# Optimization experiments

Hardware: AMD Instinct MI355X
Metric: run time of the kernel (lower is better)

The kernel has to match this reference:

```python
import jax, jax.numpy as jnp
import numpy as np

NUM_HEADS = 16
HEAD_DIM = 64
HIDDEN = NUM_HEADS * HEAD_DIM  # 1024
MAX_POS = 1024


def setup_inputs() -> dict:
    key = jax.random.key(0)
    ks = jax.random.split(key, 6)
    B, L, H = 8, 1024, HIDDEN
    hidden_states = jax.random.normal(ks[0], (B, L, H), dtype=jnp.float32)
    attention_mask = jnp.zeros((B, 1, 1, L), dtype=jnp.float32)
    scale = 0.02  # keep pre-softmax logits in a sane range
    Wq = jax.random.normal(ks[1], (H, H), dtype=jnp.float32) * scale
    Wk = jax.random.normal(ks[2], (H, H), dtype=jnp.float32) * scale
    Wv = jax.random.normal(ks[3], (H, H), dtype=jnp.float32) * scale
    bq = jnp.zeros((H,), dtype=jnp.float32)
    bk = jnp.zeros((H,), dtype=jnp.float32)
    bv = jnp.zeros((H,), dtype=jnp.float32)
    dist_emb = jax.random.normal(ks[4], (2 * MAX_POS - 1, HEAD_DIM), dtype=jnp.float32) * scale
    return {"hidden_states": hidden_states, "attention_mask": attention_mask,
            "Wq": Wq, "bq": bq, "Wk": Wk, "bk": bk, "Wv": Wv, "bv": bv,
            "dist_emb": dist_emb}


def _split_heads(x):
    # [B, L, H] -> [B, nH, L, hd]
    B, L, _ = x.shape
    return x.reshape(B, L, NUM_HEADS, HEAD_DIM).transpose(0, 2, 1, 3)


def reference(hidden_states, attention_mask, Wq, bq, Wk, bk, Wv, bv, dist_emb):
    B, L, H = hidden_states.shape
    q = _split_heads(hidden_states @ Wq.T + bq)  # [B,h,L,d]
    k = _split_heads(hidden_states @ Wk.T + bk)
    v = _split_heads(hidden_states @ Wv.T + bv)

    scores = jnp.einsum("bhld,bhrd->bhlr", q, k)

    # relative_key_query positional bias
    pos_l = jnp.arange(L)[:, None]
    pos_r = jnp.arange(L)[None, :]
    dist_idx = pos_l - pos_r + MAX_POS - 1          # [L, L], in [0, 2*MAX_POS-2]
    pos_emb = dist_emb[dist_idx]                    # [L, L, d]
    scores = scores + jnp.einsum("bhld,lrd->bhlr", q, pos_emb)
    scores = scores + jnp.einsum("bhrd,lrd->bhlr", k, pos_emb)

    scores = scores / jnp.sqrt(jnp.float32(HEAD_DIM))
    scores = scores + attention_mask                # additive mask broadcast [B,1,1,L]
    probs = jax.nn.softmax(scores, axis=-1)         # dropout = identity (eval)
    ctx = jnp.einsum("bhlr,bhrd->bhld", probs, v)
    ctx = ctx.transpose(0, 2, 1, 3).reshape(B, L, H)
    return ctx
```

## Files before the change

kernel.cpp:

```cpp
#include <hip/hip_runtime.h>
#include <stdint.h>

typedef short s16x8 __attribute__((ext_vector_type(8)));
typedef float f32x4 __attribute__((ext_vector_type(4)));

#define MFMA16(a, b, c) __builtin_amdgcn_mfma_f32_16x16x32_bf16((a), (b), (c), 0, 0, 0)

__device__ __forceinline__ ushort f2b(float f) {
  union { float f; uint32_t u; } x; x.f = f;
  uint32_t r = x.u + 0x7fffu + ((x.u >> 16) & 1u);
  return (ushort)(r >> 16);
}
__device__ __forceinline__ float b2f(ushort s) {
  union { uint32_t u; float f; } x; x.u = ((uint32_t)s) << 16;
  return x.f;
}
__device__ __forceinline__ uint32_t pack2t(float a, float b) {
  return __builtin_amdgcn_perm(__float_as_uint(b), __float_as_uint(a), 0x07060302u);
}
__device__ __forceinline__ uint32_t cvtpk(float a, float b) {
  uint32_t r;
  asm("v_cvt_pk_bf16_f32 %0, %1, %2" : "=v"(r) : "v"(a), "v"(b));
  return r;
}

__global__ __launch_bounds__(256) void cast_f32_bf16(const float* __restrict__ src,
                                                     ushort* __restrict__ dst, int n) {
  int i = (blockIdx.x * 256 + threadIdx.x) * 4;
  if (i + 4 <= n) {
    float4 v = *(const float4*)(src + i);
    ushort4 o; o.x = f2b(v.x); o.y = f2b(v.y); o.z = f2b(v.z); o.w = f2b(v.w);
    *(ushort4*)(dst + i) = o;
  }
}

__device__ __forceinline__ void gload16(const void* g, void* l) {
  __builtin_amdgcn_global_load_lds((const __attribute__((address_space(1))) void*)g,
                                   (__attribute__((address_space(3))) void*)l, 16, 0, 0);
}

__global__ __launch_bounds__(256) void qkv_gemm(
    const ushort* __restrict__ hb, const ushort* __restrict__ wb,
    const float* __restrict__ bq, const float* __restrict__ bk, const float* __restrict__ bv,
    ushort* __restrict__ qb, ushort* __restrict__ kb, ushort* __restrict__ vt) {
  __shared__ ushort As[128 * 32];
  __shared__ ushort Bs[128 * 32];
  const int tid = threadIdx.x;
  const int w = tid >> 6, lane = tid & 63, quad = lane >> 4, l16 = lane & 15;
  const int m0 = blockIdx.y * 128, n0 = blockIdx.x * 128;

  const int srow = w * 32 + (lane >> 2);
  const int scol = (lane & 3) * 8;
  const ushort* ga = hb + (size_t)(m0 + srow) * 1024 + scol;
  const ushort* gw = wb + (size_t)(n0 + srow) * 1024 + scol;
  ushort* lA0 = As + (w * 32) * 32;
  ushort* lA1 = As + (w * 32 + 16) * 32;
  ushort* lB0 = Bs + (w * 32) * 32;
  ushort* lB1 = Bs + (w * 32 + 16) * 32;

  f32x4 acc[4][4];
#pragma unroll
  for (int mt = 0; mt < 4; ++mt)
#pragma unroll
    for (int nt = 0; nt < 4; ++nt) acc[mt][nt] = (f32x4){0.f, 0.f, 0.f, 0.f};

  const int wm = (w >> 1) * 64, wn = (w & 1) * 64;

  for (int k0 = 0; k0 < 1024; k0 += 32) {
    gload16(ga + k0, lA0);
    gload16(ga + k0 + 16 * 1024, lA1);
    gload16(gw + k0, lB0);
    gload16(gw + k0 + 16 * 1024, lB1);
    __syncthreads();
    s16x8 af[4], bfr[4];
#pragma unroll
    for (int mt = 0; mt < 4; ++mt)
      af[mt] = *(const s16x8*)(As + (wm + 16 * mt + l16) * 32 + quad * 8);
#pragma unroll
    for (int nt = 0; nt < 4; ++nt)
      bfr[nt] = *(const s16x8*)(Bs + (wn + 16 * nt + l16) * 32 + quad * 8);
#pragma unroll
    for (int mt = 0; mt < 4; ++mt)
#pragma unroll
      for (int nt = 0; nt < 4; ++nt)
        acc[mt][nt] = MFMA16(af[mt], bfr[nt], acc[mt][nt]);
    __syncthreads();
  }

  const int mat = n0 >> 10;
  const float* bias = (mat == 0) ? bq : ((mat == 1) ? bk : bv);
  const int b = m0 >> 10;
#pragma unroll
  for (int mt = 0; mt < 4; ++mt) {
    int mbase = m0 + wm + 16 * mt + 4 * quad;
#pragma unroll
    for (int nt = 0; nt < 4; ++nt) {
      int n = n0 + wn + 16 * nt + l16;
      int o = n & 1023; int hh = o >> 6; int d = o & 63;
      float bsv = bias[o];
#pragma unroll
      for (int reg = 0; reg < 4; ++reg) {
        int l = (mbase + reg) & 1023;
        ushort bx = f2b(acc[mt][nt][reg] + bsv);
        if (mat == 0)      qb[(((size_t)(b * 16 + hh)) * 1024 + l) * 64 + d] = bx;
        else if (mat == 1) kb[(((size_t)(b * 16 + hh)) * 1024 + l) * 64 + d] = bx;
        else               vt[(((size_t)(b * 16 + hh)) * 64 + d) * 1024 + l] = bx;
      }
    }
  }
}

#define KR  0
#define VR  8192
#define ER  16384
#define SER 28672
#define PR  35072

__global__ __launch_bounds__(256, 2) void attn_kernel(
    const ushort* __restrict__ qb, const ushort* __restrict__ kb,
    const ushort* __restrict__ vt, const ushort* __restrict__ eb,
    const float* __restrict__ mask, float* __restrict__ out) {
  __shared__ __align__(16) ushort sm[39168];
  const int tid = threadIdx.x;
  const int w = tid >> 6, lane = tid & 63, quad = lane >> 4, l16 = lane & 15;
  const int bh = blockIdx.y, b = bh >> 4, h = bh & 15;
  const int l0 = blockIdx.x * 64;

  const int srow = lane >> 3;
  const int colb = ((lane & 7) ^ srow) * 8;
  const int row0 = w * 8 + srow;

  const ushort* kp = kb + ((size_t)bh * 1024 + row0) * 64 + colb;
  const ushort* vp = vt + ((size_t)bh * 64 + row0) * 1024 + colb;
  const float* maskp = mask + b * 1024 + l16;

  const int p0 = blockIdx.x % 3;

  {
    const ushort* qp = qb + ((size_t)bh * 1024 + l0 + row0) * 64 + colb;
    gload16(qp,         sm + PR + w * 512);
    gload16(qp + 2048,  sm + PR + 2048 + w * 512);
    gload16(kp,         sm + KR + w * 512);
    gload16(kp + 2048,  sm + KR + 2048 + w * 512);
    gload16(vp,         sm + VR + w * 512);
    gload16(vp + 32768, sm + VR + 2048 + w * 512);
    const int t0i = l0 + 960;
#pragma unroll
    for (int c2 = 0; c2 < 4; ++c2) {
      int jb = w * 8 + 32 * c2;
      int seg = p0 + (jb >> 6); if (seg >= 3) seg -= 3;
      int t = t0i + jb + srow; if (t > 2046) t = 2046;
      gload16(eb + (size_t)t * 64 + colb, sm + ER + seg * 4096 + (jb & 63) * 64);
    }
  }

  const int lm7 = l16 & 7;
  const int swzq = (quad ^ lm7) * 8;
  int offR0[4], offR1[4];
#pragma unroll
  for (int nt = 0; nt < 4; ++nt) {
    offR0[nt] = (16 * nt + l16) * 64 + swzq;
    offR1[nt] = offR0[nt] ^ 32;
  }
  const int offW0 = (w * 16 + l16) * 64 + swzq;
  const int offW1 = offW0 ^ 32;
  const int offPW0 = PR + offW0, offPW1 = PR + offW1;
  int eoffA[5], eoffB[5]; bool selA[5], selB[5];
#pragma unroll
  for (int i = 0; i < 5; ++i) {
    int ba = w + i, bbk = 3 - w + i;
    eoffA[i] = ((ba & 3) * 16 + l16) * 64 + swzq;  selA[i] = (ba & 4) != 0;
    eoffB[i] = ((bbk & 3) * 16 + l16) * 64 + swzq; selB[i] = (bbk & 4) != 0;
  }
  int offSW[5];
#pragma unroll
  for (int i = 0; i < 5; ++i)
    offSW[i] = SER + w * 1600 + (16 * i + l16) * 20 + 4 * quad;
  const int bbF = SER + (w * 16 + 4 * quad + 15 - l16) * 20 + l16;
  int addrP[4][4];
#pragma unroll
  for (int nt = 0; nt < 4; ++nt)
#pragma unroll
    for (int reg = 0; reg < 4; ++reg)
      addrP[nt][reg] = PR + (w * 16 + 4 * quad + reg) * 64
                     + (((2 * nt + (l16 >> 3)) ^ ((4 * quad + reg) & 7)) * 8) + lm7;
  int bidx[4]; bool bcnd[4];
#pragma unroll
  for (int r = 0; r < 4; ++r) {
    bidx[r] = (quad * 16 + ((4 * quad + r + 15 - l16) & 15)) * 4;
    bcnd[r] = (4 * quad + r) > l16;
  }

  __syncthreads();

  const s16x8 aq0 = *(const s16x8*)(sm + offPW0);
  const s16x8 aq1 = *(const s16x8*)(sm + offPW1);

  float rsum[4];
  f32x4 o_acc[4];
#pragma unroll
  for (int r = 0; r < 4; ++r) rsum[r] = 0.f;
#pragma unroll
  for (int nt = 0; nt < 4; ++nt) o_acc[nt] = (f32x4){0.f, 0.f, 0.f, 0.f};
  const f32x4 ZACC = {0.f, 0.f, 0.f, 0.f};

  const float LOG2E = 1.44269504088896f;
  const float SC = 0.125f * LOG2E;

  int s0 = p0;

#define ATTN_ITER(P)                                                               \
  {                                                                                \
    const int it = 2 * ith + (P);                                                  \
    const int r0 = it * 64;                                                        \
    __syncthreads();      \
                   \
    {                                                                              \
      const int rn = (r0 + 64) & 1023;                                             \
      gload16(kp + rn * 64,        sm + KR + 4096 * (1 - (P)) + w * 512);          \
      gload16(kp + rn * 64 + 2048, sm + KR + 4096 * (1 - (P)) + 2048 + w * 512);   \
      gload16(vp + rn,             sm + VR + 4096 * (1 - (P)) + w * 512);          \
      gload16(vp + rn + 32768,     sm + VR + 4096 * (1 - (P)) + 2048 + w * 512);   \
      int pnew = s0 + 2; if (pnew >= 3) pnew -= 3;                                 \
      const int tb = l0 + 960 - r0 - 64;                                           \
      _Pragma("unroll")                                                            \
      for (int c2 = 0; c2 < 2; ++c2) {                                             \
        int o = w * 8 + 32 * c2;                                                   \
        int t = tb + o + srow; t = t < 0 ? 0 : (t > 2046 ? 2046 : t);              \
        gload16(eb + (size_t)t * 64 + colb, sm + ER + pnew * 4096 + o * 64);       \
      }                                                                            \
    }                                                                              \
    float mkv[4];                                                                  \
    _Pragma("unroll")                                                              \
    for (int nt = 0; nt < 4; ++nt) mkv[nt] = maskp[r0 + 16 * nt] * LOG2E;          \
    const int sA4 = s0 * 4096;                                                     \
    int sBi = s0 + 1; if (sBi >= 3) sBi -= 3;                                      \
    const int sB4 = sBi * 4096;                                                    \
    const ushort* KbP = sm + KR + 4096 * (P);                                      \
                         \
    __builtin_amdgcn_s_setprio(1);                                                 \
    f32x4 zv[4];                                                                   \
    _Pragma("unroll")                                                              \
    for (int nt = 0; nt < 4; ++nt) {                                               \
      s16x8 bk0 = *(const s16x8*)(KbP + offR0[nt]);                                \
      s16x8 bk1 = *(const s16x8*)(KbP + offR1[nt]);                                \
      f32x4 z = MFMA16(aq0, bk0, ZACC);                                            \
      zv[nt] = MFMA16(aq1, bk1, z);                                                \
    }                                                                              \
    const s16x8 ak0 = *(const s16x8*)(KbP + offW0);                                \
    const s16x8 ak1 = *(const s16x8*)(KbP + offW1);                                \
    f32x4 d1[5];                                                                   \
    _Pragma("unroll")                                                              \
    for (int i = 0; i < 5; ++i) {                                                  \
      int ea = (selA[i] ? sB4 : sA4) + eoffA[i];                                   \
      s16x8 be0 = *(const s16x8*)(sm + ER + ea);                                   \
      s16x8 be1 = *(const s16x8*)(sm + ER + (ea ^ 32));                            \
      f32x4 z = MFMA16(aq0, be0, ZACC);                                            \
      d1[i] = MFMA16(aq1, be1, z);                                                 \
    }                                                                              \
    __builtin_amdgcn_s_setprio(0);                                                 \
                                  \
    _Pragma("unroll")                                                              \
    for (int r = 0; r < 4; ++r) {                                                  \
      float bp[5];                                                                 \
      _Pragma("unroll")                                                            \
      for (int i = 0; i < 5; ++i)                                                  \
        bp[i] = __int_as_float(                                                    \
            __builtin_amdgcn_ds_bpermute(bidx[r], __float_as_int(d1[i][r])));      \
      _Pragma("unroll")                                                            \
      for (int nt = 0; nt < 4; ++nt)                                               \
        zv[nt][r] += bcnd[r] ? bp[4 - nt] : bp[3 - nt];                            \
    }                                                                              \
                               \
    __builtin_amdgcn_s_setprio(1);                                                 \
    _Pragma("unroll")                                                              \
    for (int i = 0; i < 5; ++i) {                                                  \
      int ea = (selB[i] ? sB4 : sA4) + eoffB[i];                                   \
      s16x8 be0 = *(const s16x8*)(sm + ER + ea);                                   \
      s16x8 be1 = *(const s16x8*)(sm + ER + (ea ^ 32));                            \
      f32x4 z = MFMA16(ak0, be0, ZACC);                                            \
      z = MFMA16(ak1, be1, z);                                                     \
      uint2 pk; pk.x = pack2t(z[0], z[1]); pk.y = pack2t(z[2], z[3]);              \
      *(uint2*)(sm + offSW[i]) = pk;                                               \
    }                                                                              \
    __builtin_amdgcn_s_setprio(0);                                                 \
    __syncthreads();                  \
                    \
    _Pragma("unroll")                                                              \
    for (int nt = 0; nt < 4; ++nt) {                                               \
      _Pragma("unroll")                                                            \
      for (int reg = 0; reg < 4; ++reg) {                                          \
        float z2 = (zv[nt][reg] + b2f(sm[bbF + nt * 1600 + reg * 20])) * SC        \
                 + mkv[nt];                                                        \
        float pe = exp2f(z2);                                                      \
        zv[nt][reg] = pe;                                                          \
        rsum[reg] += pe;                                                           \
      }                                                                            \
    }                                                                              \
               \
    _Pragma("unroll")                                                              \
    for (int nt = 0; nt < 4; ++nt) {                                               \
      uint32_t u01 = cvtpk(zv[nt][0], zv[nt][1]);                                  \
      uint32_t u23 = cvtpk(zv[nt][2], zv[nt][3]);                                  \
      sm[addrP[nt][0]] = (ushort)u01;                                              \
      sm[addrP[nt][1]] = (ushort)(u01 >> 16);                                      \
      sm[addrP[nt][2]] = (ushort)u23;                                              \
      sm[addrP[nt][3]] = (ushort)(u23 >> 16);                                      \
    }                                                                              \
       \
    __builtin_amdgcn_s_setprio(1);                                                 \
    {                                                                              \
      const ushort* VbP = sm + VR + 4096 * (P);                                    \
      const s16x8 ap0 = *(const s16x8*)(sm + offPW0);                              \
      _Pragma("unroll")                                                            \
      for (int nt = 0; nt < 4; ++nt) {                                             \
        s16x8 bv0 = *(const s16x8*)(VbP + offR0[nt]);                              \
        o_acc[nt] = MFMA16(ap0, bv0, o_acc[nt]);                                   \
      }                                                                            \
      const s16x8 ap1 = *(const s16x8*)(sm + offPW1);                              \
      _Pragma("unroll")                                                            \
      for (int nt = 0; nt < 4; ++nt) {                                             \
        s16x8 bv1 = *(const s16x8*)(VbP + offR1[nt]);                              \
        o_acc[nt] = MFMA16(ap1, bv1, o_acc[nt]);                                   \
      }                                                                            \
    }                                                                              \
    __builtin_amdgcn_s_setprio(0);                                                 \
    s0 = (s0 == 0) ? 2 : s0 - 1;                   \
  }

#pragma unroll 1
  for (int ith = 0; ith < 8; ++ith) {
    ATTN_ITER(0)
    ATTN_ITER(1)
  }
#undef ATTN_ITER

#pragma unroll
  for (int off = 1; off < 16; off <<= 1)
#pragma unroll
    for (int reg = 0; reg < 4; ++reg)
      rsum[reg] += __shfl_xor(rsum[reg], off);

#pragma unroll
  for (int nt = 0; nt < 4; ++nt)
#pragma unroll
    for (int reg = 0; reg < 4; ++reg) {
      int l = l0 + w * 16 + 4 * quad + reg;
      int d = 16 * nt + l16;
      out[((size_t)(b * 1024 + l)) * 1024 + h * 64 + d] = o_acc[nt][reg] / rsum[reg];
    }
}

extern "C" void kernel_launch(void* const* d_in, const int* in_sizes, int n_in,
                              void* d_out, int out_size, void* d_ws, size_t ws_size,
                              hipStream_t stream) {
  const float* hidden = (const float*)d_in[0];
  const float* mask   = (const float*)d_in[1];
  const float* Wq     = (const float*)d_in[2];
  const float* bq     = (const float*)d_in[3];
  const float* Wk     = (const float*)d_in[4];
  const float* bk     = (const float*)d_in[5];
  const float* Wv     = (const float*)d_in[6];
  const float* bv     = (const float*)d_in[7];
  const float* dist   = (const float*)d_in[8];
  float* out = (float*)d_out;

  ushort* ws = (ushort*)d_ws;
  ushort* qb = ws;
  ushort* kb = ws + 8388608;
  ushort* vt = ws + 16777216;
  ushort* hb = ws + 25165824;
  ushort* wb = ws + 33554432;
  ushort* eb = ws + 36700160;

  cast_f32_bf16<<<8192, 256, 0, stream>>>(hidden, hb, 8388608);
  cast_f32_bf16<<<1024, 256, 0, stream>>>(Wq, wb, 1048576);
  cast_f32_bf16<<<1024, 256, 0, stream>>>(Wk, wb + 1048576, 1048576);
  cast_f32_bf16<<<1024, 256, 0, stream>>>(Wv, wb + 2097152, 1048576);
  cast_f32_bf16<<<128, 256, 0, stream>>>(dist, eb, 131008);

  qkv_gemm<<<dim3(24, 64), 256, 0, stream>>>(hb, wb, bq, bk, bv, qb, kb, vt);
  attn_kernel<<<dim3(16, 128), 256, 0, stream>>>(qb, kb, vt, eb, mask, out);
}
```

Before: 382.7 us.

## Double-buffer QKV GEMM LDS tiles, use explicit waitcnt barriers, merge weight casts

The QKV GEMM now uses two LDS buffers, so the global-to-LDS load of the next K slice is issued before the MFMAs on the current slice. This overlaps load latency with compute. Barriers in the GEMM and attention kernels are replaced with explicit s_waitcnt vmcnt/lgkmcnt plus s_barrier, and the barrier at the first attention iteration is skipped. These barriers rely on the waits being correct for the async LDS loads. The three weight cast launches are merged into one kernel to cut launch overhead.

```diff
diff --git a/kernel.cpp b/kernel.cpp
--- a/kernel.cpp
+++ b/kernel.cpp
@@ -22,6 +22,17 @@
   uint32_t r;
   asm("v_cvt_pk_bf16_f32 %0, %1, %2" : "=v"(r) : "v"(a), "v"(b));
   return r;
+}
+
+__device__ __forceinline__ void barrier_vm() {
+  asm volatile("s_waitcnt vmcnt(0)" ::: "memory");
+  __builtin_amdgcn_s_barrier();
+  __builtin_amdgcn_sched_barrier(0);
+}
+__device__ __forceinline__ void barrier_lgkm() {
+  asm volatile("s_waitcnt lgkmcnt(0)" ::: "memory");
+  __builtin_amdgcn_s_barrier();
+  __builtin_amdgcn_sched_barrier(0);
 }
 
 __global__ __launch_bounds__(256) void cast_f32_bf16(const float* __restrict__ src,
@@ -34,6 +45,20 @@
   }
 }
 
+__global__ __launch_bounds__(256) void cast3_f32_bf16(
+    const float* __restrict__ a, const float* __restrict__ b,
+    const float* __restrict__ c, ushort* __restrict__ dst) {
+  int blk = blockIdx.x;
+  const float* src; int base;
+  if (blk < 1024)      { src = a; base = 0; }
+  else if (blk < 2048) { src = b; base = 1048576; blk -= 1024; }
+  else                 { src = c; base = 2097152; blk -= 2048; }
+  int i = (blk * 256 + threadIdx.x) * 4;
+  float4 v = *(const float4*)(src + i);
+  ushort4 o; o.x = f2b(v.x); o.y = f2b(v.y); o.z = f2b(v.z); o.w = f2b(v.w);
+  *(ushort4*)(dst + base + i) = o;
+}
+
 __device__ __forceinline__ void gload16(const void* g, void* l) {
   __builtin_amdgcn_global_load_lds((const __attribute__((address_space(1))) void*)g,
                                    (__attribute__((address_space(3))) void*)l, 16, 0, 0);
@@ -43,8 +68,8 @@
     const ushort* __restrict__ hb, const ushort* __restrict__ wb,
     const float* __restrict__ bq, const float* __restrict__ bk, const float* __restrict__ bv,
     ushort* __restrict__ qb, ushort* __restrict__ kb, ushort* __restrict__ vt) {
-  __shared__ ushort As[128 * 32];
-  __shared__ ushort Bs[128 * 32];
+  __shared__ ushort As[2][4096];
+  __shared__ ushort Bs[2][4096];
   const int tid = threadIdx.x;
   const int w = tid >> 6, lane = tid & 63, quad = lane >> 4, l16 = lane & 15;
   const int m0 = blockIdx.y * 128, n0 = blockIdx.x * 128;
@@ -53,10 +78,6 @@
   const int scol = (lane & 3) * 8;
   const ushort* ga = hb + (size_t)(m0 + srow) * 1024 + scol;
   const ushort* gw = wb + (size_t)(n0 + srow) * 1024 + scol;
-  ushort* lA0 = As + (w * 32) * 32;
-  ushort* lA1 = As + (w * 32 + 16) * 32;
-  ushort* lB0 = Bs + (w * 32) * 32;
-  ushort* lB1 = Bs + (w * 32 + 16) * 32;
 
   f32x4 acc[4][4];
 #pragma unroll
@@ -66,26 +87,40 @@
 
   const int wm = (w >> 1) * 64, wn = (w & 1) * 64;
 
-  for (int k0 = 0; k0 < 1024; k0 += 32) {
-    gload16(ga + k0, lA0);
-    gload16(ga + k0 + 16 * 1024, lA1);
-    gload16(gw + k0, lB0);
-    gload16(gw + k0 + 16 * 1024, lB1);
-    __syncthreads();
-    s16x8 af[4], bfr[4];
-#pragma unroll
-    for (int mt = 0; mt < 4; ++mt)
-      af[mt] = *(const s16x8*)(As + (wm + 16 * mt + l16) * 32 + quad * 8);
-#pragma unroll
-    for (int nt = 0; nt < 4; ++nt)
-      bfr[nt] = *(const s16x8*)(Bs + (wn + 16 * nt + l16) * 32 + quad * 8);
-#pragma unroll
-    for (int mt = 0; mt < 4; ++mt)
-#pragma unroll
-      for (int nt = 0; nt < 4; ++nt)
-        acc[mt][nt] = MFMA16(af[mt], bfr[nt], acc[mt][nt]);
-    __syncthreads();
-  }
+#define STAGE(C, K0)                                          \
+  gload16(ga + (K0), As[C] + w * 1024);                       \
+  gload16(ga + (K0) + 16 * 1024, As[C] + w * 1024 + 512);     \
+  gload16(gw + (K0), Bs[C] + w * 1024);                       \
+  gload16(gw + (K0) + 16 * 1024, Bs[C] + w * 1024 + 512);
+
+#define COMPUTE(C)                                                           \
+  {                                                                          \
+    s16x8 af[4], bfr[4];                                                     \
+    _Pragma("unroll")                                                        \
+    for (int mt = 0; mt < 4; ++mt)                                           \
+      af[mt] = *(const s16x8*)(As[C] + (wm + 16 * mt + l16) * 32 + quad * 8);\
+    _Pragma("unroll")                                                        \
+    for (int nt = 0; nt < 4; ++nt)                                           \
+      bfr[nt] = *(const s16x8*)(Bs[C] + (wn + 16 * nt + l16) * 32 + quad * 8);\
+    _Pragma("unroll")                                                        \
+    for (int mt = 0; mt < 4; ++mt)                                           \
+      _Pragma("unroll")                                                      \
+      for (int nt = 0; nt < 4; ++nt)                                         \
+        acc[mt][nt] = MFMA16(af[mt], bfr[nt], acc[mt][nt]);                  \
+  }
+
+  STAGE(0, 0)
+#pragma unroll 1
+  for (int t2 = 0; t2 < 16; ++t2) {
+    barrier_vm();
+    STAGE(1, t2 * 64 + 32)
+    COMPUTE(0)
+    barrier_vm();
+    if (t2 < 15) { STAGE(0, t2 * 64 + 64) }
+    COMPUTE(1)
+  }
+#undef STAGE
+#undef COMPUTE
 
   const int mat = n0 >> 10;
   const float* bias = (mat == 0) ? bq : ((mat == 1) ? bk : bv);
@@ -191,7 +226,7 @@
     bcnd[r] = (4 * quad + r) > l16;
   }
 
-  __syncthreads();
+  barrier_vm();
 
   const s16x8 aq0 = *(const s16x8*)(sm + offPW0);
   const s16x8 aq1 = *(const s16x8*)(sm + offPW1);
@@ -213,8 +248,8 @@
   {                                                                                \
     const int it = 2 * ith + (P);                                                  \
     const int r0 = it * 64;                                                        \
-    __syncthreads();      \
-                   \
+    if (it > 0) barrier_vm();     \
+          \
     {                                                                              \
       const int rn = (r0 + 64) & 1023;                                             \
       gload16(kp + rn * 64,        sm + KR + 4096 * (1 - (P)) + w * 512);          \
@@ -284,7 +319,7 @@
       *(uint2*)(sm + offSW[i]) = pk;                                               \
     }                                                                              \
     __builtin_amdgcn_s_setprio(0);                                                 \
-    __syncthreads();                  \
+    barrier_lgkm();                   \
                     \
     _Pragma("unroll")                                                              \
     for (int nt = 0; nt < 4; ++nt) {                                               \
@@ -374,9 +409,7 @@
   ushort* eb = ws + 36700160;
 
   cast_f32_bf16<<<8192, 256, 0, stream>>>(hidden, hb, 8388608);
-  cast_f32_bf16<<<1024, 256, 0, stream>>>(Wq, wb, 1048576);
-  cast_f32_bf16<<<1024, 256, 0, stream>>>(Wk, wb + 1048576, 1048576);
-  cast_f32_bf16<<<1024, 256, 0, stream>>>(Wv, wb + 2097152, 1048576);
+  cast3_f32_bf16<<<3072, 256, 0, stream>>>(Wq, Wk, Wv, wb);
   cast_f32_bf16<<<128, 256, 0, stream>>>(dist, eb, 131008);
 
   qkv_gemm<<<dim3(24, 64), 256, 0, stream>>>(hb, wb, bq, bk, bv, qb, kb, vt);
```

Result: no change. 389.5 us (+1.8%).
